# Performance work log

Measured on AMD Instinct MI355X. Metric: run time of the kernel, lower is better.

## Reference

```python
import jax, jax.numpy as jnp
import numpy as np

D = 256  # input_dim


def setup_inputs() -> dict:
    key = jax.random.key(0)
    ks = jax.random.split(key, 10)
    s = 1.0 / np.sqrt(D)  # torch Linear init scale (uniform bound)
    desc0 = jax.random.normal(ks[0], (4, 4096, D), dtype=jnp.float32)
    desc1 = jax.random.normal(ks[1], (4, 4096, D), dtype=jnp.float32)
    def lin(kw, kb):
        W = jax.random.uniform(kw, (D, D), jnp.float32, -s, s)
        b = jax.random.uniform(kb, (D,), jnp.float32, -s, s)
        return W, b
    Wq, bq = lin(ks[2], ks[3])
    Wk, bk = lin(ks[4], ks[5])
    Wv, bv = lin(ks[6], ks[7])
    Wo, bo = lin(ks[8], ks[9])
    return {"desc0": desc0, "desc1": desc1,
            "Wq": Wq, "bq": bq, "Wk": Wk, "bk": bk,
            "Wv": Wv, "bv": bv, "Wo": Wo, "bo": bo}


def reference(desc0, desc1, Wq, bq, Wk, bk, Wv, bv, Wo, bo):
    # torch Linear: y = x @ W.T + b
    q = desc0 @ Wq.T + bq                      # [B, N0, D]
    k = desc1 @ Wk.T + bk                      # [B, N1, D]
    v = desc1 @ Wv.T + bv                      # [B, N1, D]
    scale = 1.0 / jnp.sqrt(jnp.asarray(q.shape[-1], q.dtype))
    attn = jnp.einsum('bqd,bkd->bqk', q, k) * scale  # [B, N0, N1]
    weights = jax.nn.softmax(attn, axis=-1)
    out = jnp.einsum('bqk,bkd->bqd', weights, v)     # [B, N0, D]
    return out @ Wo.T + bo
```

## Files before the change

kernel.cpp:

```cpp
#include <hip/hip_runtime.h>


typedef __attribute__((ext_vector_type(8))) __bf16 bf16x8;
typedef __attribute__((ext_vector_type(4))) float f32x4;
typedef __attribute__((ext_vector_type(16))) float f32x16;
typedef __attribute__((ext_vector_type(4))) unsigned int u32x4;
typedef __attribute__((ext_vector_type(2))) unsigned int u32x2;
typedef __attribute__((ext_vector_type(4))) unsigned short us16x4;

__device__ __forceinline__ unsigned short f2bf(float f) {
  unsigned u = __builtin_bit_cast(unsigned, f);
  u += 0x7FFFu + ((u >> 16) & 1u);
  return (unsigned short)(u >> 16);
}
__device__ __forceinline__ unsigned pk2(float a, float b) {
  return (unsigned)f2bf(a) | ((unsigned)f2bf(b) << 16);
}
__device__ __forceinline__ unsigned cvtpk(float lo, float hi) {
  unsigned r;
  asm("v_cvt_pk_bf16_f32 %0, %1, %2" : "=v"(r) : "v"(lo), "v"(hi));
  return r;
}
__device__ __forceinline__ float bf2f(unsigned short s) {
  return __builtin_bit_cast(float, ((unsigned)s) << 16);
}
__device__ __forceinline__ int swz4(int r) { return (r ^ (r >> 2)) & 3; }
__device__ __forceinline__ bf16x8 ldbf16(const void* p) {
  return __builtin_bit_cast(bf16x8, *(const u32x4*)p);
}
__device__ __forceinline__ f32x4 mfma16(bf16x8 a, bf16x8 b, f32x4 c) {
  return __builtin_amdgcn_mfma_f32_16x16x32_bf16(a, b, c, 0, 0, 0);
}
__device__ __forceinline__ f32x16 mfma32(bf16x8 a, bf16x8 b, f32x16 c) {
  return __builtin_amdgcn_mfma_f32_32x32x16_bf16(a, b, c, 0, 0, 0);
}
__device__ __forceinline__ void gld16(void* lds, const void* gsrc) {
  __builtin_amdgcn_global_load_lds(
      (const __attribute__((address_space(1))) unsigned int*)gsrc,
      (__attribute__((address_space(3))) unsigned int*)lds, 16, 0, 0);
}

__global__ __launch_bounds__(256, 4) void qkv_k(
    const float* __restrict__ desc0, const float* __restrict__ desc1,
    const float* __restrict__ Wq, const float* __restrict__ bq,
    const float* __restrict__ Wk, const float* __restrict__ bk,
    const float* __restrict__ Wv, const float* __restrict__ bv,
    unsigned short* __restrict__ qout, unsigned short* __restrict__ kout,
    unsigned short* __restrict__ vout) {
  __shared__ __align__(16) unsigned short Al[2][64 * 32];
  __shared__ __align__(16) unsigned short W1l[2][64 * 32];
  __shared__ __align__(16) unsigned short W2l[2][64 * 32];
  __shared__ float b1l[64], b2l[64];
  const int tid = threadIdx.x;
  const int w = tid >> 6, l = tid & 63, g = l >> 4, c = l & 15;
  const int bid = blockIdx.x;
  const bool iskv = bid >= 1024;
  const int bb = iskv ? bid - 1024 : bid;
  const int mt = bb & 255, nq = bb >> 8;
  const int row0 = mt * 64, n0 = nq * 64;
  const float* A = iskv ? desc1 : desc0;
  const float* W1 = iskv ? Wk : Wq;
  if (tid < 64) {
    b1l[tid] = (iskv ? bk : bq)[n0 + tid];
    if (iskv) b2l[tid] = bv[n0 + tid];
  }

  const int sr = tid >> 2, seg = tid & 3;
  const int ssw = swz4(sr);

#define CONV8(dst, X, Y)                                                              \
  {                                                                                   \
    u32x4 _v;                                                                         \
    _v[0] = pk2((X).x, (X).y); _v[1] = pk2((X).z, (X).w);                             \
    _v[2] = pk2((Y).x, (Y).y); _v[3] = pk2((Y).z, (Y).w);                             \
    *(u32x4*)(dst) = _v;                                                              \
  }

  {
    const float* ap = A + (size_t)(row0 + sr) * 256 + seg * 8;
    float4 ax = *(const float4*)ap, ay = *(const float4*)(ap + 4);
    CONV8(&Al[0][sr * 32 + ((seg ^ ssw) << 3)], ax, ay);
    const float* wp = W1 + (size_t)(n0 + sr) * 256 + seg * 8;
    float4 wx = *(const float4*)wp, wy = *(const float4*)(wp + 4);
    CONV8(&W1l[0][sr * 32 + ((seg ^ ssw) << 3)], wx, wy);
    if (iskv) {
      const float* wp2 = Wv + (size_t)(n0 + sr) * 256 + seg * 8;
      float4 w2x = *(const float4*)wp2, w2y = *(const float4*)(wp2 + 4);
      CONV8(&W2l[0][sr * 32 + ((seg ^ ssw) << 3)], w2x, w2y);
    }
  }
  __syncthreads();

  f32x4 acc1[4], acc2[4];
#pragma unroll
  for (int jt = 0; jt < 4; ++jt) {
    acc1[jt] = (f32x4){0.f, 0.f, 0.f, 0.f};
    acc2[jt] = (f32x4){0.f, 0.f, 0.f, 0.f};
  }

#pragma unroll 1
  for (int ch = 0; ch < 8; ++ch) {
    const int cur = ch & 1;
    const bool pre = (ch + 1 < 8);
    float4 ax, ay, wx, wy, w2x, w2y;
    if (pre) {
      const int ko = (ch + 1) * 32 + seg * 8;
      const float* ap = A + (size_t)(row0 + sr) * 256 + ko;
      ax = *(const float4*)ap; ay = *(const float4*)(ap + 4);
      const float* wp = W1 + (size_t)(n0 + sr) * 256 + ko;
      wx = *(const float4*)wp; wy = *(const float4*)(wp + 4);
      if (iskv) {
        const float* wp2 = Wv + (size_t)(n0 + sr) * 256 + ko;
        w2x = *(const float4*)wp2; w2y = *(const float4*)(wp2 + 4);
      }
    }
    const int ra = w * 16 + c;
    bf16x8 af = ldbf16(&Al[cur][ra * 32 + ((g ^ swz4(ra)) << 3)]);
#pragma unroll
    for (int jt = 0; jt < 4; ++jt) {
      const int j = jt * 16 + c;
      bf16x8 w1f = ldbf16(&W1l[cur][j * 32 + ((g ^ swz4(j)) << 3)]);
      acc1[jt] = mfma16(af, w1f, acc1[jt]);
    }
    if (iskv) {
#pragma unroll
      for (int jt = 0; jt < 4; ++jt) {
        const int j = jt * 16 + c;
        bf16x8 w2f = ldbf16(&W2l[cur][j * 32 + ((g ^ swz4(j)) << 3)]);
        acc2[jt] = mfma16(af, w2f, acc2[jt]);
      }
    }
    if (pre) {
      CONV8(&Al[1 - cur][sr * 32 + ((seg ^ ssw) << 3)], ax, ay);
      CONV8(&W1l[1 - cur][sr * 32 + ((seg ^ ssw) << 3)], wx, wy);
      if (iskv) CONV8(&W2l[1 - cur][sr * 32 + ((seg ^ ssw) << 3)], w2x, w2y);
    }
    __syncthreads();
  }
#undef CONV8

  unsigned short* o1 = iskv ? kout : qout;
  const int rloc = w * 16 + (g << 2);
#pragma unroll
  for (int jt = 0; jt < 4; ++jt) {
    const int col = n0 + jt * 16 + c;
    const float bvv = b1l[jt * 16 + c];
#pragma unroll
    for (int r = 0; r < 4; ++r)
      o1[(size_t)(row0 + rloc + r) * 256 + col] = f2bf(acc1[jt][r] + bvv);
  }
  if (iskv) {
    const int n = row0 + rloc;
    const int b = n >> 12, nl = n & 4095;
#pragma unroll
    for (int jt = 0; jt < 4; ++jt) {
      const int col = n0 + jt * 16 + c;
      const float bvv = b2l[jt * 16 + c];
      us16x4 pk;
      pk[0] = f2bf(acc2[jt][0] + bvv); pk[1] = f2bf(acc2[jt][1] + bvv);
      pk[2] = f2bf(acc2[jt][2] + bvv); pk[3] = f2bf(acc2[jt][3] + bvv);
      *(us16x4*)(vout + (size_t)b * 1048576 + (size_t)(nl >> 6) * 16384 + col * 64 + (nl & 63)) = pk;
    }
  }
}

template <int IN_MODE>
__global__ __launch_bounds__(256, 4) void projo_k(const unsigned short* __restrict__ Ain,
                                                  const float* __restrict__ W,
                                                  const float* __restrict__ bias,
                                                  float* __restrict__ Cout,
                                                  const float* __restrict__ lwA) {
  __shared__ __align__(16) unsigned short Al[2][64 * 32];
  __shared__ __align__(16) unsigned short Wl[2][64 * 32];
  __shared__ float biasl[64];
  const int tid = threadIdx.x;
  const int w = tid >> 6, l = tid & 63, g = l >> 4, c = l & 15;
  const int mt = blockIdx.x & 255, nq = blockIdx.x >> 8;
  const int row0 = mt * 64, n0 = nq * 64;
  if (tid < 64) biasl[tid] = bias[n0 + tid];

  const int sr = tid >> 2, seg = tid & 3;
  const int ssw = swz4(sr);

  float ainv;
  {
    const int grow = row0 + sr;
    float lt = lwA[grow];
    if (IN_MODE == 2) lt += lwA[16384 + grow];
    ainv = 1.f / lt;
  }

#define ACONV(dst, M0, M1)                                                          \
  {                                                                                 \
    u32x4 _v;                                                                       \
    _Pragma("unroll") for (int i = 0; i < 4; ++i) {                                 \
      float _lo = bf2f((unsigned short)((M0)[i] & 0xFFFF));                         \
      float _hi = bf2f((unsigned short)((M0)[i] >> 16));                            \
      if (IN_MODE == 2) {                                                           \
        _lo += bf2f((unsigned short)((M1)[i] & 0xFFFF));                            \
        _hi += bf2f((unsigned short)((M1)[i] >> 16));                               \
      }                                                                             \
      _v[i] = pk2(_lo * ainv, _hi * ainv);                                          \
    }                                                                               \
    *(u32x4*)(dst) = _v;                                                            \
  }

  {
    const unsigned short* ap = Ain + (size_t)(row0 + sr) * 256 + seg * 8;
    u32x4 a0 = *(const u32x4*)ap;
    u32x4 a1 = (IN_MODE == 2) ? *(const u32x4*)(ap + 4194304) : a0;
    ACONV(&Al[0][sr * 32 + ((seg ^ ssw) << 3)], a0, a1);
    const float* wp = W + (size_t)(n0 + sr) * 256 + seg * 8;
    float4 x = *(const float4*)wp, y = *(const float4*)(wp + 4);
    u32x4 v; v[0] = pk2(x.x, x.y); v[1] = pk2(x.z, x.w); v[2] = pk2(y.x, y.y); v[3] = pk2(y.z, y.w);
    *(u32x4*)&Wl[0][sr * 32 + ((seg ^ ssw) << 3)] = v;
  }
  __syncthreads();

  f32x4 acc[4];
#pragma unroll
  for (int jt = 0; jt < 4; ++jt) acc[jt] = (f32x4){0.f, 0.f, 0.f, 0.f};

#pragma unroll 1
  for (int ch = 0; ch < 8; ++ch) {
    const int cur = ch & 1;
    const bool pre = (ch + 1 < 8);
    float4 wx, wy; u32x4 abv, abv2;
    if (pre) {
      const int ko = (ch + 1) * 32 + seg * 8;
      const unsigned short* ap = Ain + (size_t)(row0 + sr) * 256 + ko;
      abv = *(const u32x4*)ap;
      if (IN_MODE == 2) abv2 = *(const u32x4*)(ap + 4194304);
      const float* wp = W + (size_t)(n0 + sr) * 256 + ko;
      wx = *(const float4*)wp; wy = *(const float4*)(wp + 4);
    }
    const int ra = w * 16 + c;
    bf16x8 af = ldbf16(&Al[cur][ra * 32 + ((g ^ swz4(ra)) << 3)]);
#pragma unroll
    for (int jt = 0; jt < 4; ++jt) {
      const int j = jt * 16 + c;
      bf16x8 bfr = ldbf16(&Wl[cur][j * 32 + ((g ^ swz4(j)) << 3)]);
      acc[jt] = mfma16(af, bfr, acc[jt]);
    }
    if (pre) {
      ACONV(&Al[1 - cur][sr * 32 + ((seg ^ ssw) << 3)], abv, abv2);
      u32x4 vw; vw[0] = pk2(wx.x, wx.y); vw[1] = pk2(wx.z, wx.w); vw[2] = pk2(wy.x, wy.y); vw[3] = pk2(wy.z, wy.w);
      *(u32x4*)&Wl[1 - cur][sr * 32 + ((seg ^ ssw) << 3)] = vw;
    }
    __syncthreads();
  }
#undef ACONV

#pragma unroll
  for (int jt = 0; jt < 4; ++jt) {
    const int col = n0 + jt * 16 + c;
    const float bv = biasl[jt * 16 + c];
    const int rloc = w * 16 + (g << 2);
#pragma unroll
    for (int r = 0; r < 4; ++r)
      Cout[(size_t)(row0 + rloc + r) * 256 + col] = acc[jt][r] + bv;
  }
}

template <int NS>
__global__ __launch_bounds__(512, 2) void attn_k(const unsigned short* __restrict__ qg,
                                                 const unsigned short* __restrict__ kg,
                                                 const unsigned short* __restrict__ vg,
                                                 unsigned short* __restrict__ part,
                                                 float* __restrict__ lw) {
  __shared__ __align__(16) unsigned char smem[148480];
  const int tid = threadIdx.x, w = tid >> 6, l = tid & 63;
  const int l31 = l & 31, h5 = l >> 5;
  const int qt = w >> 1, hf = w & 1;
  const int dh = w >> 1, qh = w & 1;
  const int bid = blockIdx.x;
  const int b4 = bid & 3;
  const int s = (NS == 2) ? ((bid >> 2) & 1) : 0;
  const int qtl = (NS == 2) ? (bid >> 3) : (bid >> 2);
  const int q0 = qtl * 128;
  const int NT = (NS == 2) ? 32 : 64;

  const unsigned short* kb = kg + (size_t)b4 * 1048576 + (size_t)s * 524288;
  const unsigned short* vb = vg + (size_t)b4 * 1048576 + (size_t)s * 32 * 16384;

  bf16x8 qf[16];
  {
    const unsigned short* qp = qg + ((size_t)b4 * 4096 + q0 + qt * 32 + l31) * 256;
#pragma unroll
    for (int kst = 0; kst < 16; ++kst) qf[kst] = ldbf16(qp + kst * 16 + h5 * 8);
  }

  f32x16 o[4];
#pragma unroll
  for (int d = 0; d < 4; ++d)
#pragma unroll
    for (int r = 0; r < 16; ++r) o[d][r] = 0.f;
  float l_run = 0.f;

  int goffK[4], goffV[4];
#pragma unroll
  for (int i = 0; i < 4; ++i) {
    const int sl = i * 512 + tid;
    const int kk = sl >> 5, ch = sl & 31;
    goffK[i] = kk * 256 + ((ch ^ (kk & 31)) << 3);
    const int r = sl >> 4, p16 = sl & 15;
    const int x = p16 ^ (r & 15);
    goffV[i] = (2 * r + (x >> 3)) * 64 + ((x & 7) << 3);
  }
#define STAGE(buf, t1)                                                                   \
  {                                                                                      \
    const unsigned short* _ks = kb + (size_t)(t1) * 16384;                               \
    const unsigned short* _vs = vb + (size_t)(t1) * 16384;                               \
    _Pragma("unroll") for (int i = 0; i < 4; ++i)                                        \
        gld16(smem + (buf) * 32768 + i * 8192 + w * 1024, _ks + goffK[i]);               \
    _Pragma("unroll") for (int i = 0; i < 4; ++i)                                        \
        gld16(smem + 65536 + (buf) * 32768 + i * 8192 + w * 1024, _vs + goffV[i]);       \
  }

  STAGE(0, 0);
  __syncthreads();

  const float alpha = 0.09016844f;
  unsigned char* Pq = smem + 131072 + qt * 4096;
  const int kkr = hf * 32 + l31;

#pragma unroll 1
  for (int t = 0; t < NT; ++t) {
    const int cur = t & 1;
    if (t + 1 < NT) STAGE(1 - cur, t + 1);

    const unsigned char* Kc = smem + cur * 32768 + kkr * 512;
    f32x16 sa, sb;
#pragma unroll
    for (int r = 0; r < 16; ++r) { sa[r] = 0.f; sb[r] = 0.f; }
    __builtin_amdgcn_s_setprio(1);
#pragma unroll
    for (int kst = 0; kst < 16; ++kst) {
      bf16x8 kf = ldbf16(Kc + (((kst * 2 + h5) ^ l31) << 4));
      if (kst & 1) sb = mfma32(kf, qf[kst], sb);
      else         sa = mfma32(kf, qf[kst], sa);
    }
    __builtin_amdgcn_s_setprio(0);

    float p[16];
#pragma unroll
    for (int r = 0; r < 16; ++r) p[r] = exp2f((sa[r] + sb[r]) * alpha);
    float ls = ((p[0] + p[1]) + (p[2] + p[3])) + ((p[4] + p[5]) + (p[6] + p[7])) +
               (((p[8] + p[9]) + (p[10] + p[11])) + ((p[12] + p[13]) + (p[14] + p[15])));
    l_run += ls;

    unsigned u[8];
#pragma unroll
    for (int i = 0; i < 8; ++i) u[i] = cvtpk(p[2 * i], p[2 * i + 1]);
#pragma unroll
    for (int j = 0; j < 4; ++j) {
      u32x2 dv; dv[0] = u[2 * j]; dv[1] = u[2 * j + 1];
      *(u32x2*)(Pq + l31 * 128 + (((j + 4 * hf) ^ (l31 & 7)) << 4) + h5 * 8) = dv;
    }

    asm volatile("s_waitcnt lgkmcnt(0)\n\ts_barrier" ::: "memory");
    __builtin_amdgcn_sched_barrier(0);

    const unsigned char* Vc = smem + 65536 + cur * 32768;
    bf16x8 va[8];
#pragma unroll
    for (int dd = 0; dd < 2; ++dd) {
      const int dm = dh * 64 + dd * 32 + l31;
      const int rr = dm >> 1;
      const unsigned char* Vr = Vc + rr * 256;
      const int xb = (dm & 1) * 8;
#pragma unroll
      for (int kst = 0; kst < 4; ++kst)
        va[dd * 4 + kst] = ldbf16(Vr + (((xb + kst * 2 + h5) ^ (rr & 15)) << 4));
    }
    __builtin_amdgcn_s_setprio(1);
#pragma unroll
    for (int qq = 0; qq < 2; ++qq) {
      const unsigned char* Pr = smem + 131072 + (qh * 2 + qq) * 4096;
      bf16x8 pb[4];
#pragma unroll
      for (int kst = 0; kst < 4; ++kst)
        pb[kst] = ldbf16(Pr + l31 * 128 + (((kst * 2 + h5) ^ (l31 & 7)) << 4));
#pragma unroll
      for (int dd = 0; dd < 2; ++dd)
#pragma unroll
        for (int kst = 0; kst < 4; ++kst)
          o[dd * 2 + qq] = mfma32(va[dd * 4 + kst], pb[kst], o[dd * 2 + qq]);
    }
    __builtin_amdgcn_s_setprio(0);

    __syncthreads();
  }
#undef STAGE

  l_run += __shfl_xor(l_run, 32);

  float* Lb = (float*)(smem + 147456);
  if (l < 32) Lb[(qt * 2 + hf) * 32 + l31] = l_run;
  __syncthreads();

  unsigned char* T = smem + w * 16384;
#pragma unroll
  for (int dd = 0; dd < 2; ++dd)
#pragma unroll
    for (int qq = 0; qq < 2; ++qq)
#pragma unroll
      for (int rg = 0; rg < 4; ++rg) {
        f32x4 wv;
        wv[0] = o[dd * 2 + qq][4 * rg + 0]; wv[1] = o[dd * 2 + qq][4 * rg + 1];
        wv[2] = o[dd * 2 + qq][4 * rg + 2]; wv[3] = o[dd * 2 + qq][4 * rg + 3];
        const int qloc = qq * 32 + l31;
        const int c16 = dd * 8 + rg * 2 + h5;
        *(f32x4*)(T + qloc * 256 + ((c16 ^ (qloc & 15)) << 4)) = wv;
      }
  asm volatile("s_waitcnt lgkmcnt(0)" ::: "memory");
  __builtin_amdgcn_sched_barrier(0);
  {
    const int qloc = l;
    f32x4 rv[16];
#pragma unroll
    for (int c16 = 0; c16 < 16; ++c16)
      rv[c16] = *(const f32x4*)(T + qloc * 256 + ((c16 ^ (qloc & 15)) << 4));
    unsigned short* op = part + (size_t)s * 4194304 +
                         ((size_t)b4 * 4096 + q0 + qh * 64 + qloc) * 256 + dh * 64;
#pragma unroll
    for (int i = 0; i < 8; ++i) {
      u32x4 ov;
      ov[0] = pk2(rv[2 * i][0], rv[2 * i][1]);
      ov[1] = pk2(rv[2 * i][2], rv[2 * i][3]);
      ov[2] = pk2(rv[2 * i + 1][0], rv[2 * i + 1][1]);
      ov[3] = pk2(rv[2 * i + 1][2], rv[2 * i + 1][3]);
      *(u32x4*)(op + i * 8) = ov;
    }
  }
  if (hf == 0 && l < 32) {
    const float lt = Lb[(qt * 2) * 32 + l31] + Lb[(qt * 2 + 1) * 32 + l31];
    lw[(size_t)s * 16384 + (size_t)b4 * 4096 + q0 + qt * 32 + l31] = lt;
  }
}

extern "C" void kernel_launch(void* const* d_in, const int* in_sizes, int n_in,
                              void* d_out, int out_size, void* d_ws, size_t ws_size,
                              hipStream_t stream) {
  (void)in_sizes; (void)n_in; (void)out_size;
  const float* desc0 = (const float*)d_in[0];
  const float* desc1 = (const float*)d_in[1];
  const float* Wq = (const float*)d_in[2];
  const float* bq = (const float*)d_in[3];
  const float* Wk = (const float*)d_in[4];
  const float* bk = (const float*)d_in[5];
  const float* Wv = (const float*)d_in[6];
  const float* bv = (const float*)d_in[7];
  const float* Wo = (const float*)d_in[8];
  const float* bo = (const float*)d_in[9];

  unsigned char* ws = (unsigned char*)d_ws;
  unsigned short* qw = (unsigned short*)(ws);
  unsigned short* kw = (unsigned short*)(ws + 8388608);
  unsigned short* vw = (unsigned short*)(ws + 16777216);
  unsigned short* part = (unsigned short*)(ws + 25165824);
  float* lwp = (float*)(ws + 41943040);

  const bool two = (ws_size >= 42008576ull);

  qkv_k<<<2048, 256, 0, stream>>>(desc0, desc1, Wq, bq, Wk, bk, Wv, bv, qw, kw, vw);
  if (two) {
    attn_k<2><<<256, 512, 0, stream>>>(qw, kw, vw, part, lwp);
    projo_k<2><<<1024, 256, 0, stream>>>(part, Wo, bo, (float*)d_out, lwp);
  } else {
    lwp = (float*)(ws + 33554432);
    attn_k<1><<<128, 512, 0, stream>>>(qw, kw, vw, part, lwp);
    projo_k<3><<<1024, 256, 0, stream>>>(part, Wo, bo, (float*)d_out, lwp);
  }
}
```

Baseline: 123.2 us.

## Software-pipeline PV of previous tile with QK of current tile in attention

Restructures the attention loop so the P·V product for tile t-1 runs right after the QK MFMAs for tile t, with P double-buffered in LDS. This removes the mid-iteration barrier that used to separate the softmax write of P from its consumption. V loads are now issued one tile later than K, and a final PV step is added after the loop. The cost is more LDS (up to 160KB), which limits occupancy, plus a longer dependency window for V loads.

```diff
diff --git a/kernel.cpp b/kernel.cpp
--- a/kernel.cpp
+++ b/kernel.cpp
@@ -268,7 +268,7 @@
                                                  const unsigned short* __restrict__ vg,
                                                  unsigned short* __restrict__ part,
                                                  float* __restrict__ lw) {
-  __shared__ __align__(16) unsigned char smem[148480];
+  __shared__ __align__(16) unsigned char smem[163840];
   const int tid = threadIdx.x, w = tid >> 6, l = tid & 63;
   const int l31 = l & 31, h5 = l >> 5;
   const int qt = w >> 1, hf = w & 1;
@@ -307,27 +307,54 @@
     const int x = p16 ^ (r & 15);
     goffV[i] = (2 * r + (x >> 3)) * 64 + ((x & 7) << 3);
   }
-#define STAGE(buf, t1)                                                                   \
+#define STAGEK(buf, t1)                                                                  \
   {                                                                                      \
     const unsigned short* _ks = kb + (size_t)(t1) * 16384;                               \
+    _Pragma("unroll") for (int i = 0; i < 4; ++i)                                        \
+        gld16(smem + (buf) * 32768 + i * 8192 + w * 1024, _ks + goffK[i]);               \
+  }
+#define STAGEV(buf, t1)                                                                  \
+  {                                                                                      \
     const unsigned short* _vs = vb + (size_t)(t1) * 16384;                               \
     _Pragma("unroll") for (int i = 0; i < 4; ++i)                                        \
-        gld16(smem + (buf) * 32768 + i * 8192 + w * 1024, _ks + goffK[i]);               \
-    _Pragma("unroll") for (int i = 0; i < 4; ++i)                                        \
         gld16(smem + 65536 + (buf) * 32768 + i * 8192 + w * 1024, _vs + goffV[i]);       \
   }
-
-  STAGE(0, 0);
+#define PVBODY(pbuf)                                                                     \
+  {                                                                                      \
+    const unsigned char* Vc = smem + 65536 + (pbuf) * 32768;                             \
+    bf16x8 va[8];                                                                        \
+    _Pragma("unroll") for (int dd = 0; dd < 2; ++dd) {                                   \
+      const int dm = dh * 64 + dd * 32 + l31;                                            \
+      const int rr = dm >> 1;                                                            \
+      const unsigned char* Vr = Vc + rr * 256;                                           \
+      const int xb = (dm & 1) * 8;                                                       \
+      _Pragma("unroll") for (int kst = 0; kst < 4; ++kst)                                \
+          va[dd * 4 + kst] = ldbf16(Vr + (((xb + kst * 2 + h5) ^ (rr & 15)) << 4));      \
+    }                                                                                    \
+    __builtin_amdgcn_s_setprio(1);                                                       \
+    _Pragma("unroll") for (int qq = 0; qq < 2; ++qq) {                                   \
+      const unsigned char* Pr = smem + 131072 + (pbuf) * 16384 + (qh * 2 + qq) * 4096;   \
+      bf16x8 pb[4];                                                                      \
+      _Pragma("unroll") for (int kst = 0; kst < 4; ++kst)                                \
+          pb[kst] = ldbf16(Pr + l31 * 128 + (((kst * 2 + h5) ^ (l31 & 7)) << 4));        \
+      _Pragma("unroll") for (int dd = 0; dd < 2; ++dd)                                   \
+          _Pragma("unroll") for (int kst = 0; kst < 4; ++kst)                            \
+              o[dd * 2 + qq] = mfma32(va[dd * 4 + kst], pb[kst], o[dd * 2 + qq]);        \
+    }                                                                                    \
+    __builtin_amdgcn_s_setprio(0);                                                       \
+  }
+
+  STAGEK(0, 0);
   __syncthreads();
 
   const float alpha = 0.09016844f;
-  unsigned char* Pq = smem + 131072 + qt * 4096;
   const int kkr = hf * 32 + l31;
 
 #pragma unroll 1
   for (int t = 0; t < NT; ++t) {
     const int cur = t & 1;
-    if (t + 1 < NT) STAGE(1 - cur, t + 1);
+    if (t + 1 < NT) STAGEK(1 - cur, t + 1);
+    STAGEV(cur, t);
 
     const unsigned char* Kc = smem + cur * 32768 + kkr * 512;
     f32x16 sa, sb;
@@ -341,6 +368,7 @@
       else         sa = mfma32(kf, qf[kst], sa);
     }
     __builtin_amdgcn_s_setprio(0);
+    if (t > 0) PVBODY(1 - cur);
 
     float p[16];
 #pragma unroll
@@ -352,50 +380,23 @@
     unsigned u[8];
 #pragma unroll
     for (int i = 0; i < 8; ++i) u[i] = cvtpk(p[2 * i], p[2 * i + 1]);
+    unsigned char* Pq = smem + 131072 + cur * 16384 + qt * 4096;
 #pragma unroll
     for (int j = 0; j < 4; ++j) {
       u32x2 dv; dv[0] = u[2 * j]; dv[1] = u[2 * j + 1];
       *(u32x2*)(Pq + l31 * 128 + (((j + 4 * hf) ^ (l31 & 7)) << 4) + h5 * 8) = dv;
     }
 
-    asm volatile("s_waitcnt lgkmcnt(0)\n\ts_barrier" ::: "memory");
-    __builtin_amdgcn_sched_barrier(0);
-
-    const unsigned char* Vc = smem + 65536 + cur * 32768;
-    bf16x8 va[8];
-#pragma unroll
-    for (int dd = 0; dd < 2; ++dd) {
-      const int dm = dh * 64 + dd * 32 + l31;
-      const int rr = dm >> 1;
-      const unsigned char* Vr = Vc + rr * 256;
-      const int xb = (dm & 1) * 8;
-#pragma unroll
-      for (int kst = 0; kst < 4; ++kst)
-        va[dd * 4 + kst] = ldbf16(Vr + (((xb + kst * 2 + h5) ^ (rr & 15)) << 4));
-    }
-    __builtin_amdgcn_s_setprio(1);
-#pragma unroll
-    for (int qq = 0; qq < 2; ++qq) {
-      const unsigned char* Pr = smem + 131072 + (qh * 2 + qq) * 4096;
-      bf16x8 pb[4];
-#pragma unroll
-      for (int kst = 0; kst < 4; ++kst)
-        pb[kst] = ldbf16(Pr + l31 * 128 + (((kst * 2 + h5) ^ (l31 & 7)) << 4));
-#pragma unroll
-      for (int dd = 0; dd < 2; ++dd)
-#pragma unroll
-        for (int kst = 0; kst < 4; ++kst)
-          o[dd * 2 + qq] = mfma32(va[dd * 4 + kst], pb[kst], o[dd * 2 + qq]);
-    }
-    __builtin_amdgcn_s_setprio(0);
-
     __syncthreads();
   }
-#undef STAGE
+  PVBODY((NT - 1) & 1);
+#undef STAGEK
+#undef STAGEV
+#undef PVBODY
 
   l_run += __shfl_xor(l_run, 32);
 
-  float* Lb = (float*)(smem + 147456);
+  float* Lb = (float*)(smem + 131072);
   if (l < 32) Lb[(qt * 2 + hf) * 32 + l31] = l_run;
   __syncthreads();
 
```

Measured after the change: 150.4 us. +22.1%, slower.
